# Optimization experiments

Measured on AMD Instinct MI355X. Metric: run time of the kernel, lower is better.

## Reference

```python
import jax, jax.numpy as jnp
import numpy as np

EPS = 1e-12  # matches torch F.normalize eps


def _l2_normalize(x):
    n = jnp.linalg.norm(x, axis=-1, keepdims=True)
    return x / jnp.maximum(n, EPS)


def setup_inputs() -> dict:
    key = jax.random.key(0)
    k1, k2, k3 = jax.random.split(key, 3)
    N, E, D = 100000, 1200000, 64
    feat = jax.random.normal(k1, (N, D), dtype=jnp.float32)
    beta = jnp.ones((1,), dtype=jnp.float32)
    src = jax.random.randint(k2, (E,), 0, N, dtype=jnp.int32)
    dst = jax.random.randint(k3, (E,), 0, N, dtype=jnp.int32)
    return {"feat": feat, "beta": beta, "src": src, "dst": dst}


def reference(feat, beta, src, dst):
    N = feat.shape[0]
    # cosine similarity on each edge (AGNN att_type)
    nh = _l2_normalize(feat)                                  # [N, D]
    e = beta[0] * jnp.sum(nh[src] * nh[dst], axis=-1)         # [E]
    # edge softmax over incoming edges of each destination node
    emax = jax.ops.segment_max(e, dst, num_segments=N)        # [N]
    emax = jnp.where(jnp.isfinite(emax), emax, 0.0)           # isolated nodes
    p = jnp.exp(e - emax[dst])                                # [E]
    psum = jax.ops.segment_sum(p, dst, num_segments=N)        # [N]
    p = p / jnp.maximum(psum[dst], EPS)                       # [E]
    # weighted scatter-sum aggregation: h_i' = sum_j p_ij * h_j
    msg = feat[src] * p[:, None]                              # [E, D]
    out = jax.ops.segment_sum(msg, dst, num_segments=N)       # [N, D]
    return out
```

## Files before the change

### kernel.cpp

```cpp
#include <hip/hip_runtime.h>
#include <hip/hip_fp16.h>

#define D 64
#define EPS 1e-12f
#define NPB 512
#define NPB_SHIFT 9
#define NB 256
#define CAP 8192
#define CAP_SHIFT 13
#define EPB 4096
#define SRC_BITS 17

typedef _Float16 hv2 __attribute__((ext_vector_type(2)));

__device__ inline unsigned bc_u(__half2 h) { return __builtin_bit_cast(unsigned, h); }
__device__ inline __half2  bc_h(unsigned u) { return __builtin_bit_cast(__half2, u); }

__device__ inline float fdot2f(unsigned a, unsigned b, float c) {
#if defined(__has_builtin) && __has_builtin(__builtin_amdgcn_fdot2)
    return __builtin_amdgcn_fdot2(__builtin_bit_cast(hv2, a),
                                  __builtin_bit_cast(hv2, b), c, false);
#else
    __half2 ah = bc_h(a), bh = bc_h(b);
    return c + __low2float(ah) * __low2float(bh)
             + __high2float(ah) * __high2float(bh);
#endif
}

__global__ __launch_bounds__(1024) void scatter_kernel(
        const int* __restrict__ src,
        const int* __restrict__ dst,
        int* __restrict__ bincursor,
        unsigned* __restrict__ pairs, int E) {
    __shared__ int hist[NB], offs[NB], cursor[NB], gbase[NB], tmp[NB];
    __shared__ int dstbuf[EPB];
    __shared__ unsigned buf[EPB];
    __shared__ unsigned char binof[EPB];

    int tid  = threadIdx.x;
    int base = blockIdx.x * EPB;
    int cnt  = min(EPB, E - base);

    if (tid < NB) hist[tid] = 0;
    __syncthreads();
    for (int i = tid; i < cnt; i += 1024) {
        int dd = dst[base + i];
        dstbuf[i] = dd;
        atomicAdd(&hist[dd >> NPB_SHIFT], 1);
    }
    __syncthreads();
    int v = 0;
    if (tid < NB) { v = hist[tid]; tmp[tid] = v; }
    __syncthreads();
    #pragma unroll
    for (int off = 1; off < NB; off <<= 1) {
        int t = 0;
        if (tid < NB && tid >= off) t = tmp[tid - off];
        __syncthreads();
        if (tid < NB) tmp[tid] += t;
        __syncthreads();
    }
    if (tid < NB) {
        int e = tmp[tid] - v;
        offs[tid] = e; cursor[tid] = e;
        if (v > 0)
            gbase[tid] = (tid << CAP_SHIFT) + atomicAdd(&bincursor[tid], v);
    }
    __syncthreads();
    for (int i = tid; i < cnt; i += 1024) {
        int s = src[base + i], dd = dstbuf[i];
        int b = dd >> NPB_SHIFT;
        int l = atomicAdd(&cursor[b], 1);
        buf[l]   = ((unsigned)(dd & (NPB - 1)) << SRC_BITS) | (unsigned)s;
        binof[l] = (unsigned char)b;
    }
    __syncthreads();
    for (int i = tid; i < cnt; i += 1024) {
        int b = binof[i];
        pairs[gbase[b] + (i - offs[b])] = buf[i];
    }
}

__global__ __launch_bounds__(1024) void csr_nh_kernel(
        const unsigned* __restrict__ pairs,
        const int* __restrict__ bincursor,
        int* __restrict__ rowbeg,
        int* __restrict__ rowend,
        int* __restrict__ esrc,
        const float4* __restrict__ feat4,
        float* __restrict__ norms,
        uint2* __restrict__ nh2,
        int N, int nbins) {
    __shared__ unsigned buf[CAP];
    __shared__ int hist[NPB], cursor[NPB], tmp[NPB];

    if ((int)blockIdx.x >= nbins) {
        int gid = (blockIdx.x - nbins) * 1024 + threadIdx.x;
        int row = gid >> 4;
        int lg  = gid & 15;
        if (row >= N) return;
        float4 v = feat4[row * 16 + lg];
        float ss = v.x * v.x + v.y * v.y + v.z * v.z + v.w * v.w;
        #pragma unroll
        for (int off = 1; off < 16; off <<= 1) ss += __shfl_xor(ss, off, 64);
        float nrm = fmaxf(sqrtf(ss), EPS);
        float inv = 1.0f / nrm;
        if (lg == 0) norms[row] = nrm;
        uint2 p;
        p.x = bc_u(__floats2half2_rn(v.x * inv, v.y * inv));
        p.y = bc_u(__floats2half2_rn(v.z * inv, v.w * inv));
        nh2[row * 16 + lg] = p;
        return;
    }

    int b    = blockIdx.x;
    int tid  = threadIdx.x;
    int base = b << CAP_SHIFT;
    int cnt  = bincursor[b];
    int node0 = b << NPB_SHIFT;

    if (tid < NPB) hist[tid] = 0;
    __syncthreads();
    for (int i = tid; i < cnt; i += 1024) {
        unsigned p = pairs[base + i];
        buf[i] = p;
        atomicAdd(&hist[p >> SRC_BITS], 1);
    }
    __syncthreads();
    int v = 0;
    if (tid < NPB) { v = hist[tid]; tmp[tid] = v; }
    __syncthreads();
    #pragma unroll
    for (int off = 1; off < NPB; off <<= 1) {
        int t = 0;
        if (tid < NPB && tid >= off) t = tmp[tid - off];
        __syncthreads();
        if (tid < NPB) tmp[tid] += t;
        __syncthreads();
    }
    if (tid < NPB) {
        int excl = tmp[tid] - v;
        cursor[tid] = excl;
        int node = node0 + tid;
        if (node < N) { rowbeg[node] = base + excl; rowend[node] = base + excl + v; }
    }
    __syncthreads();
    for (int i = tid; i < cnt; i += 1024) {
        unsigned p = buf[i];
        int pos = atomicAdd(&cursor[p >> SRC_BITS], 1);
        esrc[base + pos] = (int)(p & ((1u << SRC_BITS) - 1));
    }
}

__global__ __launch_bounds__(256) void gather_kernel(const uint4* __restrict__ nh4,
                                                     const float* __restrict__ norms,
                                                     const float* __restrict__ beta_p,
                                                     const int* __restrict__ rowbeg,
                                                     const int* __restrict__ rowend,
                                                     const int* __restrict__ esrc,
                                                     float4* __restrict__ out4, int N) {
    int t    = blockIdx.x * 256 + threadIdx.x;
    int lane = threadIdx.x & 63;
    int g    = lane >> 3;
    int lg   = lane & 7;
    int d    = (t >> 6) * 8 + g;
    if (d >= N) return;

    int j   = rowbeg[d];
    int end = rowend[d];
    float beta = beta_p[0];

    uint4 fdp = nh4[(size_t)d * 8 + lg];

    __half2 acc0 = __float2half2_rn(0.f), acc1 = acc0, acc2 = acc0, acc3 = acc0;
    float ps = 0.f;

    for (; j < end; j += 4) {
        bool v1 = (j + 1 < end), v2 = (j + 2 < end), v3 = (j + 3 < end);
        int s0 = esrc[j];
        int s1 = v1 ? esrc[j + 1] : s0;
        int s2 = v2 ? esrc[j + 2] : s0;
        int s3 = v3 ? esrc[j + 3] : s0;
        uint4 p0 = nh4[(size_t)s0 * 8 + lg];
        uint4 p1 = nh4[(size_t)s1 * 8 + lg];
        uint4 p2 = nh4[(size_t)s2 * 8 + lg];
        uint4 p3 = nh4[(size_t)s3 * 8 + lg];
        float n0 = norms[s0], n1 = norms[s1], n2 = norms[s2], n3 = norms[s3];
        float d0 = fdot2f(p0.x, fdp.x, 0.f), d1 = fdot2f(p1.x, fdp.x, 0.f);
        float d2 = fdot2f(p2.x, fdp.x, 0.f), d3 = fdot2f(p3.x, fdp.x, 0.f);
        d0 = fdot2f(p0.y, fdp.y, d0); d1 = fdot2f(p1.y, fdp.y, d1);
        d2 = fdot2f(p2.y, fdp.y, d2); d3 = fdot2f(p3.y, fdp.y, d3);
        d0 = fdot2f(p0.z, fdp.z, d0); d1 = fdot2f(p1.z, fdp.z, d1);
        d2 = fdot2f(p2.z, fdp.z, d2); d3 = fdot2f(p3.z, fdp.z, d3);
        d0 = fdot2f(p0.w, fdp.w, d0); d1 = fdot2f(p1.w, fdp.w, d1);
        d2 = fdot2f(p2.w, fdp.w, d2); d3 = fdot2f(p3.w, fdp.w, d3);
        #pragma unroll
        for (int off = 1; off < 8; off <<= 1) {
            d0 += __shfl_xor(d0, off, 64);
            d1 += __shfl_xor(d1, off, 64);
            d2 += __shfl_xor(d2, off, 64);
            d3 += __shfl_xor(d3, off, 64);
        }
        float w0 = __expf(beta * d0);
        float w1 = v1 ? __expf(beta * d1) : 0.f;
        float w2 = v2 ? __expf(beta * d2) : 0.f;
        float w3 = v3 ? __expf(beta * d3) : 0.f;
        __half2 q0 = __float2half2_rn(w0 * n0);
        __half2 q1 = __float2half2_rn(w1 * n1);
        __half2 q2 = __float2half2_rn(w2 * n2);
        __half2 q3 = __float2half2_rn(w3 * n3);
        acc0 = __hfma2(q0, bc_h(p0.x), acc0); acc0 = __hfma2(q1, bc_h(p1.x), acc0);
        acc0 = __hfma2(q2, bc_h(p2.x), acc0); acc0 = __hfma2(q3, bc_h(p3.x), acc0);
        acc1 = __hfma2(q0, bc_h(p0.y), acc1); acc1 = __hfma2(q1, bc_h(p1.y), acc1);
        acc1 = __hfma2(q2, bc_h(p2.y), acc1); acc1 = __hfma2(q3, bc_h(p3.y), acc1);
        acc2 = __hfma2(q0, bc_h(p0.z), acc2); acc2 = __hfma2(q1, bc_h(p1.z), acc2);
        acc2 = __hfma2(q2, bc_h(p2.z), acc2); acc2 = __hfma2(q3, bc_h(p3.z), acc2);
        acc3 = __hfma2(q0, bc_h(p0.w), acc3); acc3 = __hfma2(q1, bc_h(p1.w), acc3);
        acc3 = __hfma2(q2, bc_h(p2.w), acc3); acc3 = __hfma2(q3, bc_h(p3.w), acc3);
        ps += w0 + w1 + w2 + w3;
    }

    float r = 1.0f / fmaxf(ps, EPS);
    float4 o0 = {__low2float(acc0) * r, __high2float(acc0) * r,
                 __low2float(acc1) * r, __high2float(acc1) * r};
    float4 o1 = {__low2float(acc2) * r, __high2float(acc2) * r,
                 __low2float(acc3) * r, __high2float(acc3) * r};
    out4[(size_t)d * 16 + lg * 2]     = o0;
    out4[(size_t)d * 16 + lg * 2 + 1] = o1;
}

extern "C" void kernel_launch(void* const* d_in, const int* in_sizes, int n_in,
                              void* d_out, int out_size, void* d_ws, size_t ws_size,
                              hipStream_t stream) {
    const float* feat = (const float*)d_in[0];
    const float* beta = (const float*)d_in[1];
    const int*   src  = (const int*)d_in[2];
    const int*   dst  = (const int*)d_in[3];

    int N = in_sizes[0] / D;
    int E = in_sizes[2];
    int nbins = (N + NPB - 1) / NPB;

    unsigned* pairs     = (unsigned*)d_ws;
    int*      esrc      = (int*)(pairs + (size_t)nbins * CAP);
    unsigned* nhraw     = (unsigned*)(esrc + (size_t)nbins * CAP);
    float*    norms     = (float*)(nhraw + (size_t)N * 32);
    int*      bincursor = (int*)(norms + N);
    int*      rowbeg    = bincursor + NB;
    int*      rowend    = rowbeg + N;

    hipMemsetAsync(bincursor, 0, NB * sizeof(int), stream);

    int BS = (E + EPB - 1) / EPB;
    int BI = (N * 16 + 1023) / 1024;
    scatter_kernel<<<BS, 1024, 0, stream>>>(src, dst, bincursor, pairs, E);
    csr_nh_kernel<<<nbins + BI, 1024, 0, stream>>>(
        pairs, bincursor, rowbeg, rowend, esrc,
        (const float4*)feat, norms, (uint2*)nhraw, N, nbins);
    gather_kernel<<<(N + 31) / 32, 256, 0, stream>>>(
        (const uint4*)nhraw, norms, beta, rowbeg, rowend, esrc,
        (float4*)d_out, N);
}
```

Measured before the change: 135.1 us.

## Fuse three stages into one persistent kernel with grid barriers

```diff
diff --git a/kernel.cpp b/kernel.cpp
--- a/kernel.cpp
+++ b/kernel.cpp
@@ -10,6 +10,8 @@
 #define CAP_SHIFT 13
 #define EPB 4096
 #define SRC_BITS 17
+#define GB 256
+#define BT 1024
 
 typedef _Float16 hv2 __attribute__((ext_vector_type(2)));
 
@@ -27,206 +29,241 @@
 #endif
 }
 
-__global__ __launch_bounds__(1024) void scatter_kernel(
+struct SmemP1 {
+    int dstbuf[EPB];
+    unsigned buf[EPB];
+    int hist[NB], offs[NB], cursor[NB], gbase[NB];
+    unsigned char binof[EPB];
+};
+struct SmemP2 {
+    unsigned buf[CAP];
+    int hist[NPB], cursor[NPB];
+};
+constexpr size_t SMEM_BYTES = sizeof(SmemP1) > sizeof(SmemP2) ? sizeof(SmemP1)
+                                                              : sizeof(SmemP2);
+
+__device__ inline void grid_barrier(int* cnt, int target) {
+    __syncthreads();
+    if (threadIdx.x == 0) {
+        __threadfence();
+        atomicAdd(cnt, 1);
+        while (__hip_atomic_load(cnt, __ATOMIC_RELAXED, __HIP_MEMORY_SCOPE_AGENT)
+               < target)
+            __builtin_amdgcn_s_sleep(2);
+        __threadfence();
+    }
+    __syncthreads();
+}
+
+__global__ __launch_bounds__(BT) void fused_kernel(
         const int* __restrict__ src,
         const int* __restrict__ dst,
+        const float4* __restrict__ feat4,
+        const float* __restrict__ beta_p,
+        unsigned* __restrict__ pairs,
         int* __restrict__ bincursor,
-        unsigned* __restrict__ pairs, int E) {
-    __shared__ int hist[NB], offs[NB], cursor[NB], gbase[NB], tmp[NB];
-    __shared__ int dstbuf[EPB];
-    __shared__ unsigned buf[EPB];
-    __shared__ unsigned char binof[EPB];
-
-    int tid  = threadIdx.x;
-    int base = blockIdx.x * EPB;
-    int cnt  = min(EPB, E - base);
-
-    if (tid < NB) hist[tid] = 0;
-    __syncthreads();
-    for (int i = tid; i < cnt; i += 1024) {
-        int dd = dst[base + i];
-        dstbuf[i] = dd;
-        atomicAdd(&hist[dd >> NPB_SHIFT], 1);
-    }
-    __syncthreads();
-    int v = 0;
-    if (tid < NB) { v = hist[tid]; tmp[tid] = v; }
-    __syncthreads();
-    #pragma unroll
-    for (int off = 1; off < NB; off <<= 1) {
-        int t = 0;
-        if (tid < NB && tid >= off) t = tmp[tid - off];
-        __syncthreads();
-        if (tid < NB) tmp[tid] += t;
-        __syncthreads();
-    }
-    if (tid < NB) {
-        int e = tmp[tid] - v;
-        offs[tid] = e; cursor[tid] = e;
-        if (v > 0)
-            gbase[tid] = (tid << CAP_SHIFT) + atomicAdd(&bincursor[tid], v);
-    }
-    __syncthreads();
-    for (int i = tid; i < cnt; i += 1024) {
-        int s = src[base + i], dd = dstbuf[i];
-        int b = dd >> NPB_SHIFT;
-        int l = atomicAdd(&cursor[b], 1);
-        buf[l]   = ((unsigned)(dd & (NPB - 1)) << SRC_BITS) | (unsigned)s;
-        binof[l] = (unsigned char)b;
-    }
-    __syncthreads();
-    for (int i = tid; i < cnt; i += 1024) {
-        int b = binof[i];
-        pairs[gbase[b] + (i - offs[b])] = buf[i];
-    }
-}
-
-__global__ __launch_bounds__(1024) void csr_nh_kernel(
-        const unsigned* __restrict__ pairs,
-        const int* __restrict__ bincursor,
+        int* __restrict__ barcnt,
         int* __restrict__ rowbeg,
         int* __restrict__ rowend,
         int* __restrict__ esrc,
-        const float4* __restrict__ feat4,
         float* __restrict__ norms,
         uint2* __restrict__ nh2,
-        int N, int nbins) {
-    __shared__ unsigned buf[CAP];
-    __shared__ int hist[NPB], cursor[NPB], tmp[NPB];
-
-    if ((int)blockIdx.x >= nbins) {
-        int gid = (blockIdx.x - nbins) * 1024 + threadIdx.x;
-        int row = gid >> 4;
-        int lg  = gid & 15;
-        if (row >= N) return;
-        float4 v = feat4[row * 16 + lg];
-        float ss = v.x * v.x + v.y * v.y + v.z * v.z + v.w * v.w;
-        #pragma unroll
-        for (int off = 1; off < 16; off <<= 1) ss += __shfl_xor(ss, off, 64);
-        float nrm = fmaxf(sqrtf(ss), EPS);
-        float inv = 1.0f / nrm;
-        if (lg == 0) norms[row] = nrm;
-        uint2 p;
-        p.x = bc_u(__floats2half2_rn(v.x * inv, v.y * inv));
-        p.y = bc_u(__floats2half2_rn(v.z * inv, v.w * inv));
-        nh2[row * 16 + lg] = p;
-        return;
-    }
-
-    int b    = blockIdx.x;
-    int tid  = threadIdx.x;
-    int base = b << CAP_SHIFT;
-    int cnt  = bincursor[b];
-    int node0 = b << NPB_SHIFT;
-
-    if (tid < NPB) hist[tid] = 0;
-    __syncthreads();
-    for (int i = tid; i < cnt; i += 1024) {
-        unsigned p = pairs[base + i];
-        buf[i] = p;
-        atomicAdd(&hist[p >> SRC_BITS], 1);
-    }
-    __syncthreads();
-    int v = 0;
-    if (tid < NPB) { v = hist[tid]; tmp[tid] = v; }
-    __syncthreads();
-    #pragma unroll
-    for (int off = 1; off < NPB; off <<= 1) {
-        int t = 0;
-        if (tid < NPB && tid >= off) t = tmp[tid - off];
-        __syncthreads();
-        if (tid < NPB) tmp[tid] += t;
-        __syncthreads();
-    }
-    if (tid < NPB) {
-        int excl = tmp[tid] - v;
-        cursor[tid] = excl;
-        int node = node0 + tid;
-        if (node < N) { rowbeg[node] = base + excl; rowend[node] = base + excl + v; }
-    }
-    __syncthreads();
-    for (int i = tid; i < cnt; i += 1024) {
-        unsigned p = buf[i];
-        int pos = atomicAdd(&cursor[p >> SRC_BITS], 1);
-        esrc[base + pos] = (int)(p & ((1u << SRC_BITS) - 1));
-    }
-}
-
-__global__ __launch_bounds__(256) void gather_kernel(const uint4* __restrict__ nh4,
-                                                     const float* __restrict__ norms,
-                                                     const float* __restrict__ beta_p,
-                                                     const int* __restrict__ rowbeg,
-                                                     const int* __restrict__ rowend,
-                                                     const int* __restrict__ esrc,
-                                                     float4* __restrict__ out4, int N) {
-    int t    = blockIdx.x * 256 + threadIdx.x;
-    int lane = threadIdx.x & 63;
-    int g    = lane >> 3;
-    int lg   = lane & 7;
-    int d    = (t >> 6) * 8 + g;
-    if (d >= N) return;
-
-    int j   = rowbeg[d];
-    int end = rowend[d];
-    float beta = beta_p[0];
-
-    uint4 fdp = nh4[(size_t)d * 8 + lg];
-
-    __half2 acc0 = __float2half2_rn(0.f), acc1 = acc0, acc2 = acc0, acc3 = acc0;
-    float ps = 0.f;
-
-    for (; j < end; j += 4) {
-        bool v1 = (j + 1 < end), v2 = (j + 2 < end), v3 = (j + 3 < end);
-        int s0 = esrc[j];
-        int s1 = v1 ? esrc[j + 1] : s0;
-        int s2 = v2 ? esrc[j + 2] : s0;
-        int s3 = v3 ? esrc[j + 3] : s0;
-        uint4 p0 = nh4[(size_t)s0 * 8 + lg];
-        uint4 p1 = nh4[(size_t)s1 * 8 + lg];
-        uint4 p2 = nh4[(size_t)s2 * 8 + lg];
-        uint4 p3 = nh4[(size_t)s3 * 8 + lg];
-        float n0 = norms[s0], n1 = norms[s1], n2 = norms[s2], n3 = norms[s3];
-        float d0 = fdot2f(p0.x, fdp.x, 0.f), d1 = fdot2f(p1.x, fdp.x, 0.f);
-        float d2 = fdot2f(p2.x, fdp.x, 0.f), d3 = fdot2f(p3.x, fdp.x, 0.f);
-        d0 = fdot2f(p0.y, fdp.y, d0); d1 = fdot2f(p1.y, fdp.y, d1);
-        d2 = fdot2f(p2.y, fdp.y, d2); d3 = fdot2f(p3.y, fdp.y, d3);
-        d0 = fdot2f(p0.z, fdp.z, d0); d1 = fdot2f(p1.z, fdp.z, d1);
-        d2 = fdot2f(p2.z, fdp.z, d2); d3 = fdot2f(p3.z, fdp.z, d3);
-        d0 = fdot2f(p0.w, fdp.w, d0); d1 = fdot2f(p1.w, fdp.w, d1);
-        d2 = fdot2f(p2.w, fdp.w, d2); d3 = fdot2f(p3.w, fdp.w, d3);
-        #pragma unroll
-        for (int off = 1; off < 8; off <<= 1) {
-            d0 += __shfl_xor(d0, off, 64);
-            d1 += __shfl_xor(d1, off, 64);
-            d2 += __shfl_xor(d2, off, 64);
-            d3 += __shfl_xor(d3, off, 64);
-        }
-        float w0 = __expf(beta * d0);
-        float w1 = v1 ? __expf(beta * d1) : 0.f;
-        float w2 = v2 ? __expf(beta * d2) : 0.f;
-        float w3 = v3 ? __expf(beta * d3) : 0.f;
-        __half2 q0 = __float2half2_rn(w0 * n0);
-        __half2 q1 = __float2half2_rn(w1 * n1);
-        __half2 q2 = __float2half2_rn(w2 * n2);
-        __half2 q3 = __float2half2_rn(w3 * n3);
-        acc0 = __hfma2(q0, bc_h(p0.x), acc0); acc0 = __hfma2(q1, bc_h(p1.x), acc0);
-        acc0 = __hfma2(q2, bc_h(p2.x), acc0); acc0 = __hfma2(q3, bc_h(p3.x), acc0);
-        acc1 = __hfma2(q0, bc_h(p0.y), acc1); acc1 = __hfma2(q1, bc_h(p1.y), acc1);
-        acc1 = __hfma2(q2, bc_h(p2.y), acc1); acc1 = __hfma2(q3, bc_h(p3.y), acc1);
-        acc2 = __hfma2(q0, bc_h(p0.z), acc2); acc2 = __hfma2(q1, bc_h(p1.z), acc2);
-        acc2 = __hfma2(q2, bc_h(p2.z), acc2); acc2 = __hfma2(q3, bc_h(p3.z), acc2);
-        acc3 = __hfma2(q0, bc_h(p0.w), acc3); acc3 = __hfma2(q1, bc_h(p1.w), acc3);
-        acc3 = __hfma2(q2, bc_h(p2.w), acc3); acc3 = __hfma2(q3, bc_h(p3.w), acc3);
-        ps += w0 + w1 + w2 + w3;
-    }
-
-    float r = 1.0f / fmaxf(ps, EPS);
-    float4 o0 = {__low2float(acc0) * r, __high2float(acc0) * r,
-                 __low2float(acc1) * r, __high2float(acc1) * r};
-    float4 o1 = {__low2float(acc2) * r, __high2float(acc2) * r,
-                 __low2float(acc3) * r, __high2float(acc3) * r};
-    out4[(size_t)d * 16 + lg * 2]     = o0;
-    out4[(size_t)d * 16 + lg * 2 + 1] = o1;
+        float4* __restrict__ out4,
+        int N, int E, int nbins, int nchunks) {
+    __shared__ __align__(16) unsigned char smem[SMEM_BYTES];
+    SmemP1* s1 = (SmemP1*)smem;
+    SmemP2* s2 = (SmemP2*)smem;
+    const int tid = threadIdx.x;
+    const int bid = blockIdx.x;
+
+    for (int c = bid; c < nchunks; c += GB) {
+        int base = c * EPB;
+        int cnt  = min(EPB, E - base);
+        if (tid < NB) s1->hist[tid] = 0;
+        __syncthreads();
+        for (int i = tid; i < cnt; i += BT) {
+            int dd = dst[base + i];
+            s1->dstbuf[i] = dd;
+            atomicAdd(&s1->hist[dd >> NPB_SHIFT], 1);
+        }
+        __syncthreads();
+        if (tid < 64) {
+            int i0 = tid << 2;
+            int h0 = s1->hist[i0], h1 = s1->hist[i0 + 1];
+            int h2 = s1->hist[i0 + 2], h3 = s1->hist[i0 + 3];
+            int s = h0 + h1 + h2 + h3;
+            int run = s;
+            #pragma unroll
+            for (int off = 1; off < 64; off <<= 1) {
+                int nbr = __shfl_up(run, off, 64);
+                if (tid >= off) run += nbr;
+            }
+            int acc = run - s;
+            int hh[4] = {h0, h1, h2, h3};
+            #pragma unroll
+            for (int k = 0; k < 4; k++) {
+                s1->offs[i0 + k] = acc;
+                s1->cursor[i0 + k] = acc;
+                if (hh[k] > 0)
+                    s1->gbase[i0 + k] = ((i0 + k) << CAP_SHIFT)
+                                      + atomicAdd(&bincursor[i0 + k], hh[k]);
+                acc += hh[k];
+            }
+        }
+        __syncthreads();
+        for (int i = tid; i < cnt; i += BT) {
+            int s = src[base + i], dd = s1->dstbuf[i];
+            int b = dd >> NPB_SHIFT;
+            int l = atomicAdd(&s1->cursor[b], 1);
+            s1->buf[l]   = ((unsigned)(dd & (NPB - 1)) << SRC_BITS) | (unsigned)s;
+            s1->binof[l] = (unsigned char)b;
+        }
+        __syncthreads();
+        for (int i = tid; i < cnt; i += BT) {
+            int b = s1->binof[i];
+            pairs[s1->gbase[b] + (i - s1->offs[b])] = s1->buf[i];
+        }
+        __syncthreads();
+    }
+
+    {
+        const int stride = GB * BT;
+        for (int gid = bid * BT + tid; gid < N * 16; gid += stride) {
+            int row = gid >> 4, lg = gid & 15;
+            float4 v = feat4[gid];
+            float ss = v.x * v.x + v.y * v.y + v.z * v.z + v.w * v.w;
+            #pragma unroll
+            for (int off = 1; off < 16; off <<= 1) ss += __shfl_xor(ss, off, 64);
+            float nrm = fmaxf(sqrtf(ss), EPS);
+            float inv = 1.0f / nrm;
+            if (lg == 0) norms[row] = nrm;
+            uint2 p;
+            p.x = bc_u(__floats2half2_rn(v.x * inv, v.y * inv));
+            p.y = bc_u(__floats2half2_rn(v.z * inv, v.w * inv));
+            nh2[gid] = p;
+        }
+    }
+
+    grid_barrier(barcnt, GB);
+
+    for (int b = bid; b < nbins; b += GB) {
+        int base  = b << CAP_SHIFT;
+        int cnt   = bincursor[b];
+        int node0 = b << NPB_SHIFT;
+        if (tid < NPB) s2->hist[tid] = 0;
+        __syncthreads();
+        for (int i = tid; i < cnt; i += BT) {
+            unsigned p = pairs[base + i];
+            s2->buf[i] = p;
+            atomicAdd(&s2->hist[p >> SRC_BITS], 1);
+        }
+        __syncthreads();
+        if (tid < 64) {
+            int i0 = tid << 3;
+            int h[8], s = 0;
+            #pragma unroll
+            for (int k = 0; k < 8; k++) { h[k] = s2->hist[i0 + k]; s += h[k]; }
+            int run = s;
+            #pragma unroll
+            for (int off = 1; off < 64; off <<= 1) {
+                int nbr = __shfl_up(run, off, 64);
+                if (tid >= off) run += nbr;
+            }
+            int acc = run - s;
+            #pragma unroll
+            for (int k = 0; k < 8; k++) {
+                s2->cursor[i0 + k] = acc;
+                int node = node0 + i0 + k;
+                if (node < N) {
+                    rowbeg[node] = base + acc;
+                    rowend[node] = base + acc + h[k];
+                }
+                acc += h[k];
+            }
+        }
+        __syncthreads();
+        for (int i = tid; i < cnt; i += BT) {
+            unsigned p = s2->buf[i];
+            int pos = atomicAdd(&s2->cursor[p >> SRC_BITS], 1);
+            esrc[base + pos] = (int)(p & ((1u << SRC_BITS) - 1));
+        }
+        __syncthreads();
+    }
+
+    grid_barrier(barcnt, 2 * GB);
+
+    {
+        const uint4* nh4 = (const uint4*)nh2;
+        float beta = beta_p[0];
+        int lane = tid & 63;
+        int g  = lane >> 3;
+        int lg = lane & 7;
+        int wid = (bid << 4) + (tid >> 6);
+        const int nwaves = GB * (BT >> 6);
+        int ntasks = (N + 7) >> 3;
+        for (int task = wid; task < ntasks; task += nwaves) {
+            int d = task * 8 + g;
+            if (d >= N) continue;
+            int j   = rowbeg[d];
+            int end = rowend[d];
+            uint4 fdp = nh4[(size_t)d * 8 + lg];
+            __half2 acc0 = __float2half2_rn(0.f), acc1 = acc0;
+            __half2 acc2 = acc0, acc3 = acc0;
+            float ps = 0.f;
+            for (; j < end; j += 4) {
+                bool v1 = (j + 1 < end), v2 = (j + 2 < end), v3 = (j + 3 < end);
+                int es0 = esrc[j];
+                int es1 = v1 ? esrc[j + 1] : es0;
+                int es2 = v2 ? esrc[j + 2] : es0;
+                int es3 = v3 ? esrc[j + 3] : es0;
+                uint4 p0 = nh4[(size_t)es0 * 8 + lg];
+                uint4 p1 = nh4[(size_t)es1 * 8 + lg];
+                uint4 p2 = nh4[(size_t)es2 * 8 + lg];
+                uint4 p3 = nh4[(size_t)es3 * 8 + lg];
+                float n0 = norms[es0], n1 = norms[es1];
+                float n2 = norms[es2], n3 = norms[es3];
+                float d0 = fdot2f(p0.x, fdp.x, 0.f), d1 = fdot2f(p1.x, fdp.x, 0.f);
+                float d2 = fdot2f(p2.x, fdp.x, 0.f), d3 = fdot2f(p3.x, fdp.x, 0.f);
+                d0 = fdot2f(p0.y, fdp.y, d0); d1 = fdot2f(p1.y, fdp.y, d1);
+                d2 = fdot2f(p2.y, fdp.y, d2); d3 = fdot2f(p3.y, fdp.y, d3);
+                d0 = fdot2f(p0.z, fdp.z, d0); d1 = fdot2f(p1.z, fdp.z, d1);
+                d2 = fdot2f(p2.z, fdp.z, d2); d3 = fdot2f(p3.z, fdp.z, d3);
+                d0 = fdot2f(p0.w, fdp.w, d0); d1 = fdot2f(p1.w, fdp.w, d1);
+                d2 = fdot2f(p2.w, fdp.w, d2); d3 = fdot2f(p3.w, fdp.w, d3);
+                #pragma unroll
+                for (int off = 1; off < 8; off <<= 1) {
+                    d0 += __shfl_xor(d0, off, 64);
+                    d1 += __shfl_xor(d1, off, 64);
+                    d2 += __shfl_xor(d2, off, 64);
+                    d3 += __shfl_xor(d3, off, 64);
+                }
+                float w0 = __expf(beta * d0);
+                float w1 = v1 ? __expf(beta * d1) : 0.f;
+                float w2 = v2 ? __expf(beta * d2) : 0.f;
+                float w3 = v3 ? __expf(beta * d3) : 0.f;
+                __half2 q0 = __float2half2_rn(w0 * n0);
+                __half2 q1 = __float2half2_rn(w1 * n1);
+                __half2 q2 = __float2half2_rn(w2 * n2);
+                __half2 q3 = __float2half2_rn(w3 * n3);
+                acc0 = __hfma2(q0, bc_h(p0.x), acc0); acc0 = __hfma2(q1, bc_h(p1.x), acc0);
+                acc0 = __hfma2(q2, bc_h(p2.x), acc0); acc0 = __hfma2(q3, bc_h(p3.x), acc0);
+                acc1 = __hfma2(q0, bc_h(p0.y), acc1); acc1 = __hfma2(q1, bc_h(p1.y), acc1);
+                acc1 = __hfma2(q2, bc_h(p2.y), acc1); acc1 = __hfma2(q3, bc_h(p3.y), acc1);
+                acc2 = __hfma2(q0, bc_h(p0.z), acc2); acc2 = __hfma2(q1, bc_h(p1.z), acc2);
+                acc2 = __hfma2(q2, bc_h(p2.z), acc2); acc2 = __hfma2(q3, bc_h(p3.z), acc2);
+                acc3 = __hfma2(q0, bc_h(p0.w), acc3); acc3 = __hfma2(q1, bc_h(p1.w), acc3);
+                acc3 = __hfma2(q2, bc_h(p2.w), acc3); acc3 = __hfma2(q3, bc_h(p3.w), acc3);
+                ps += w0 + w1 + w2 + w3;
+            }
+            float r = 1.0f / fmaxf(ps, EPS);
+            float4 o0 = {__low2float(acc0) * r, __high2float(acc0) * r,
+                         __low2float(acc1) * r, __high2float(acc1) * r};
+            float4 o1 = {__low2float(acc2) * r, __high2float(acc2) * r,
+                         __low2float(acc3) * r, __high2float(acc3) * r};
+            out4[(size_t)d * 16 + lg * 2]     = o0;
+            out4[(size_t)d * 16 + lg * 2 + 1] = o1;
+        }
+    }
 }
 
 extern "C" void kernel_launch(void* const* d_in, const int* in_sizes, int n_in,
@@ -239,25 +276,23 @@
 
     int N = in_sizes[0] / D;
     int E = in_sizes[2];
-    int nbins = (N + NPB - 1) / NPB;
+    int nbins   = (N + NPB - 1) / NPB;
+    int nchunks = (E + EPB - 1) / EPB;
 
     unsigned* pairs     = (unsigned*)d_ws;
     int*      esrc      = (int*)(pairs + (size_t)nbins * CAP);
     unsigned* nhraw     = (unsigned*)(esrc + (size_t)nbins * CAP);
     float*    norms     = (float*)(nhraw + (size_t)N * 32);
     int*      bincursor = (int*)(norms + N);
-    int*      rowbeg    = bincursor + NB;
+    int*      barcnt    = bincursor + NB;
+    int*      rowbeg    = barcnt + 4;
     int*      rowend    = rowbeg + N;
 
-    hipMemsetAsync(bincursor, 0, NB * sizeof(int), stream);
-
-    int BS = (E + EPB - 1) / EPB;
-    int BI = (N * 16 + 1023) / 1024;
-    scatter_kernel<<<BS, 1024, 0, stream>>>(src, dst, bincursor, pairs, E);
-    csr_nh_kernel<<<nbins + BI, 1024, 0, stream>>>(
-        pairs, bincursor, rowbeg, rowend, esrc,
-        (const float4*)feat, norms, (uint2*)nhraw, N, nbins);
-    gather_kernel<<<(N + 31) / 32, 256, 0, stream>>>(
-        (const uint4*)nhraw, norms, beta, rowbeg, rowend, esrc,
-        (float4*)d_out, N);
-}
+    hipMemsetAsync(bincursor, 0, (NB + 4) * sizeof(int), stream);
+
+    fused_kernel<<<GB, BT, 0, stream>>>(
+        src, dst, (const float4*)feat, beta,
+        pairs, bincursor, barcnt, rowbeg, rowend, esrc,
+        norms, (uint2*)nhraw, (float4*)d_out,
+        N, E, nbins, nchunks);
+}
```

After: 213.4 us. +57.9%, slower.

## Fuse CSR build into gather via per-bin claim/done flags; merge nh into scatter

Applied to the files above, without the earlier changes.

```diff
diff --git a/kernel.cpp b/kernel.cpp
--- a/kernel.cpp
+++ b/kernel.cpp
@@ -10,6 +10,8 @@
 #define CAP_SHIFT 13
 #define EPB 4096
 #define SRC_BITS 17
+#define K2T 512
+#define NPBLK 64
 
 typedef _Float16 hv2 __attribute__((ext_vector_type(2)));
 
@@ -27,79 +29,26 @@
 #endif
 }
 
-__global__ __launch_bounds__(1024) void scatter_kernel(
+__global__ __launch_bounds__(1024) void scatter_nh_kernel(
         const int* __restrict__ src,
         const int* __restrict__ dst,
+        const float4* __restrict__ feat4,
         int* __restrict__ bincursor,
-        unsigned* __restrict__ pairs, int E) {
-    __shared__ int hist[NB], offs[NB], cursor[NB], gbase[NB], tmp[NB];
-    __shared__ int dstbuf[EPB];
-    __shared__ unsigned buf[EPB];
-    __shared__ unsigned char binof[EPB];
-
-    int tid  = threadIdx.x;
-    int base = blockIdx.x * EPB;
-    int cnt  = min(EPB, E - base);
-
-    if (tid < NB) hist[tid] = 0;
-    __syncthreads();
-    for (int i = tid; i < cnt; i += 1024) {
-        int dd = dst[base + i];
-        dstbuf[i] = dd;
-        atomicAdd(&hist[dd >> NPB_SHIFT], 1);
-    }
-    __syncthreads();
-    int v = 0;
-    if (tid < NB) { v = hist[tid]; tmp[tid] = v; }
-    __syncthreads();
-    #pragma unroll
-    for (int off = 1; off < NB; off <<= 1) {
-        int t = 0;
-        if (tid < NB && tid >= off) t = tmp[tid - off];
-        __syncthreads();
-        if (tid < NB) tmp[tid] += t;
-        __syncthreads();
-    }
-    if (tid < NB) {
-        int e = tmp[tid] - v;
-        offs[tid] = e; cursor[tid] = e;
-        if (v > 0)
-            gbase[tid] = (tid << CAP_SHIFT) + atomicAdd(&bincursor[tid], v);
-    }
-    __syncthreads();
-    for (int i = tid; i < cnt; i += 1024) {
-        int s = src[base + i], dd = dstbuf[i];
-        int b = dd >> NPB_SHIFT;
-        int l = atomicAdd(&cursor[b], 1);
-        buf[l]   = ((unsigned)(dd & (NPB - 1)) << SRC_BITS) | (unsigned)s;
-        binof[l] = (unsigned char)b;
-    }
-    __syncthreads();
-    for (int i = tid; i < cnt; i += 1024) {
-        int b = binof[i];
-        pairs[gbase[b] + (i - offs[b])] = buf[i];
-    }
-}
-
-__global__ __launch_bounds__(1024) void csr_nh_kernel(
-        const unsigned* __restrict__ pairs,
-        const int* __restrict__ bincursor,
-        int* __restrict__ rowbeg,
-        int* __restrict__ rowend,
-        int* __restrict__ esrc,
-        const float4* __restrict__ feat4,
+        unsigned* __restrict__ pairs,
         float* __restrict__ norms,
         uint2* __restrict__ nh2,
-        int N, int nbins) {
-    __shared__ unsigned buf[CAP];
-    __shared__ int hist[NPB], cursor[NPB], tmp[NPB];
-
-    if ((int)blockIdx.x >= nbins) {
-        int gid = (blockIdx.x - nbins) * 1024 + threadIdx.x;
-        int row = gid >> 4;
-        int lg  = gid & 15;
-        if (row >= N) return;
-        float4 v = feat4[row * 16 + lg];
+        int N, int E, int nchunks) {
+    __shared__ unsigned buf[EPB];
+    __shared__ int hist[NB], offs[NB], cursor[NB], gbase[NB];
+    __shared__ unsigned char binof[EPB];
+
+    int tid = threadIdx.x;
+
+    if ((int)blockIdx.x >= nchunks) {
+        int gid = (blockIdx.x - nchunks) * 1024 + tid;
+        if (gid >= N * 16) return;
+        int row = gid >> 4, lg = gid & 15;
+        float4 v = feat4[gid];
         float ss = v.x * v.x + v.y * v.y + v.z * v.z + v.w * v.w;
         #pragma unroll
         for (int off = 1; off < 16; off <<= 1) ss += __shfl_xor(ss, off, 64);
@@ -109,67 +58,173 @@
         uint2 p;
         p.x = bc_u(__floats2half2_rn(v.x * inv, v.y * inv));
         p.y = bc_u(__floats2half2_rn(v.z * inv, v.w * inv));
-        nh2[row * 16 + lg] = p;
+        nh2[gid] = p;
         return;
     }
 
-    int b    = blockIdx.x;
-    int tid  = threadIdx.x;
-    int base = b << CAP_SHIFT;
-    int cnt  = bincursor[b];
-    int node0 = b << NPB_SHIFT;
-
-    if (tid < NPB) hist[tid] = 0;
+    int base = blockIdx.x * EPB;
+    int cnt  = min(EPB, E - base);
+    int cnt4 = cnt >> 2;
+    int tail = cnt & 3;
+
+    if (tid < NB) hist[tid] = 0;
+    __syncthreads();
+
+    int4 dd4 = {0, 0, 0, 0};
+    bool have = tid < cnt4;
+    if (have) {
+        dd4 = ((const int4*)(dst + base))[tid];
+        atomicAdd(&hist[dd4.x >> NPB_SHIFT], 1);
+        atomicAdd(&hist[dd4.y >> NPB_SHIFT], 1);
+        atomicAdd(&hist[dd4.z >> NPB_SHIFT], 1);
+        atomicAdd(&hist[dd4.w >> NPB_SHIFT], 1);
+    }
+    int dtail = 0;
+    if (tid < tail) {
+        dtail = dst[base + cnt4 * 4 + tid];
+        atomicAdd(&hist[dtail >> NPB_SHIFT], 1);
+    }
+    __syncthreads();
+    if (tid < 64) {
+        int i0 = tid << 2;
+        int h0 = hist[i0], h1 = hist[i0 + 1], h2 = hist[i0 + 2], h3 = hist[i0 + 3];
+        int s = h0 + h1 + h2 + h3;
+        int run = s;
+        #pragma unroll
+        for (int off = 1; off < 64; off <<= 1) {
+            int nbr = __shfl_up(run, off, 64);
+            if (tid >= off) run += nbr;
+        }
+        int acc = run - s;
+        int hh[4] = {h0, h1, h2, h3};
+        #pragma unroll
+        for (int k = 0; k < 4; k++) {
+            offs[i0 + k] = acc;
+            cursor[i0 + k] = acc;
+            if (hh[k] > 0)
+                gbase[i0 + k] = ((i0 + k) << CAP_SHIFT)
+                              + atomicAdd(&bincursor[i0 + k], hh[k]);
+            acc += hh[k];
+        }
+    }
+    __syncthreads();
+    auto place = [&](int dd, int s) {
+        int bb = dd >> NPB_SHIFT;
+        int l = atomicAdd(&cursor[bb], 1);
+        buf[l]   = ((unsigned)(dd & (NPB - 1)) << SRC_BITS) | (unsigned)s;
+        binof[l] = (unsigned char)bb;
+    };
+    if (have) {
+        int4 ss4 = ((const int4*)(src + base))[tid];
+        place(dd4.x, ss4.x); place(dd4.y, ss4.y);
+        place(dd4.z, ss4.z); place(dd4.w, ss4.w);
+    }
+    if (tid < tail) place(dtail, src[base + cnt4 * 4 + tid]);
     __syncthreads();
     for (int i = tid; i < cnt; i += 1024) {
-        unsigned p = pairs[base + i];
-        buf[i] = p;
-        atomicAdd(&hist[p >> SRC_BITS], 1);
-    }
-    __syncthreads();
-    int v = 0;
-    if (tid < NPB) { v = hist[tid]; tmp[tid] = v; }
-    __syncthreads();
-    #pragma unroll
-    for (int off = 1; off < NPB; off <<= 1) {
-        int t = 0;
-        if (tid < NPB && tid >= off) t = tmp[tid - off];
-        __syncthreads();
-        if (tid < NPB) tmp[tid] += t;
-        __syncthreads();
-    }
-    if (tid < NPB) {
-        int excl = tmp[tid] - v;
-        cursor[tid] = excl;
-        int node = node0 + tid;
-        if (node < N) { rowbeg[node] = base + excl; rowend[node] = base + excl + v; }
-    }
-    __syncthreads();
-    for (int i = tid; i < cnt; i += 1024) {
-        unsigned p = buf[i];
-        int pos = atomicAdd(&cursor[p >> SRC_BITS], 1);
-        esrc[base + pos] = (int)(p & ((1u << SRC_BITS) - 1));
+        int b = binof[i];
+        pairs[gbase[b] + (i - offs[b])] = buf[i];
     }
 }
 
-__global__ __launch_bounds__(256) void gather_kernel(const uint4* __restrict__ nh4,
-                                                     const float* __restrict__ norms,
-                                                     const float* __restrict__ beta_p,
-                                                     const int* __restrict__ rowbeg,
-                                                     const int* __restrict__ rowend,
-                                                     const int* __restrict__ esrc,
-                                                     float4* __restrict__ out4, int N) {
-    int t    = blockIdx.x * 256 + threadIdx.x;
-    int lane = threadIdx.x & 63;
-    int g    = lane >> 3;
-    int lg   = lane & 7;
-    int d    = (t >> 6) * 8 + g;
+__global__ __launch_bounds__(K2T, 8) void csr_gather_kernel(
+        const unsigned* __restrict__ pairs,
+        const int* __restrict__ bincursor,
+        int* __restrict__ claim,
+        int* __restrict__ done,
+        int* __restrict__ rowbeg,
+        int* __restrict__ rowend,
+        int* __restrict__ esrc,
+        const uint4* __restrict__ nh4,
+        const float* __restrict__ norms,
+        const float* __restrict__ beta_p,
+        float4* __restrict__ out4, int N) {
+    __shared__ unsigned buf[CAP];
+    __shared__ int hist[NPB], cursor[NPB];
+    __shared__ int sclaim;
+
+    int tid   = threadIdx.x;
+    int node0 = blockIdx.x * NPBLK;
+    int b     = node0 >> NPB_SHIFT;
+
+    if (tid == 0) sclaim = atomicCAS(&claim[b], 0, 1);
+    __syncthreads();
+
+    if (sclaim == 0) {
+        int base = b << CAP_SHIFT;
+        int cnt  = bincursor[b];
+        int bn0  = b << NPB_SHIFT;
+        hist[tid] = 0;
+        __syncthreads();
+        int cnt4 = cnt >> 2;
+        for (int i4 = tid; i4 < cnt4; i4 += K2T) {
+            uint4 p = ((const uint4*)(pairs + base))[i4];
+            *(uint4*)&buf[i4 * 4] = p;
+            atomicAdd(&hist[p.x >> SRC_BITS], 1);
+            atomicAdd(&hist[p.y >> SRC_BITS], 1);
+            atomicAdd(&hist[p.z >> SRC_BITS], 1);
+            atomicAdd(&hist[p.w >> SRC_BITS], 1);
+        }
+        for (int i = cnt4 * 4 + tid; i < cnt; i += K2T) {
+            unsigned p = pairs[base + i];
+            buf[i] = p;
+            atomicAdd(&hist[p >> SRC_BITS], 1);
+        }
+        __syncthreads();
+        if (tid < 64) {
+            int i0 = tid << 3;
+            int h[8], s = 0;
+            #pragma unroll
+            for (int k = 0; k < 8; k++) { h[k] = hist[i0 + k]; s += h[k]; }
+            int run = s;
+            #pragma unroll
+            for (int off = 1; off < 64; off <<= 1) {
+                int nbr = __shfl_up(run, off, 64);
+                if (tid >= off) run += nbr;
+            }
+            int acc = run - s;
+            #pragma unroll
+            for (int k = 0; k < 8; k++) {
+                cursor[i0 + k] = acc;
+                int node = bn0 + i0 + k;
+                if (node < N) {
+                    rowbeg[node] = base + acc;
+                    rowend[node] = base + acc + h[k];
+                }
+                acc += h[k];
+            }
+        }
+        __syncthreads();
+        for (int i = tid; i < cnt; i += K2T) {
+            unsigned p = buf[i];
+            int pos = atomicAdd(&cursor[p >> SRC_BITS], 1);
+            esrc[base + pos] = (int)(p & ((1u << SRC_BITS) - 1));
+        }
+        __syncthreads();
+        if (tid == 0) {
+            __threadfence();
+            __hip_atomic_store(&done[b], 1, __ATOMIC_RELEASE,
+                               __HIP_MEMORY_SCOPE_AGENT);
+        }
+    } else {
+        if (tid == 0) {
+            while (__hip_atomic_load(&done[b], __ATOMIC_ACQUIRE,
+                                     __HIP_MEMORY_SCOPE_AGENT) == 0)
+                __builtin_amdgcn_s_sleep(2);
+            __threadfence();
+        }
+        __syncthreads();
+    }
+
+    int lane = tid & 63;
+    int g  = lane >> 3;
+    int lg = lane & 7;
+    int d  = node0 + (tid >> 6) * 8 + g;
     if (d >= N) return;
 
     int j   = rowbeg[d];
     int end = rowend[d];
     float beta = beta_p[0];
-
     uint4 fdp = nh4[(size_t)d * 8 + lg];
 
     __half2 acc0 = __float2half2_rn(0.f), acc1 = acc0, acc2 = acc0, acc3 = acc0;
@@ -239,25 +294,27 @@
 
     int N = in_sizes[0] / D;
     int E = in_sizes[2];
-    int nbins = (N + NPB - 1) / NPB;
+    int nbins   = (N + NPB - 1) / NPB;
+    int nchunks = (E + EPB - 1) / EPB;
 
     unsigned* pairs     = (unsigned*)d_ws;
     int*      esrc      = (int*)(pairs + (size_t)nbins * CAP);
     unsigned* nhraw     = (unsigned*)(esrc + (size_t)nbins * CAP);
     float*    norms     = (float*)(nhraw + (size_t)N * 32);
     int*      bincursor = (int*)(norms + N);
-    int*      rowbeg    = bincursor + NB;
+    int*      claim     = bincursor + NB;
+    int*      done      = claim + NB;
+    int*      rowbeg    = done + NB;
     int*      rowend    = rowbeg + N;
 
-    hipMemsetAsync(bincursor, 0, NB * sizeof(int), stream);
-
-    int BS = (E + EPB - 1) / EPB;
-    int BI = (N * 16 + 1023) / 1024;
-    scatter_kernel<<<BS, 1024, 0, stream>>>(src, dst, bincursor, pairs, E);
-    csr_nh_kernel<<<nbins + BI, 1024, 0, stream>>>(
-        pairs, bincursor, rowbeg, rowend, esrc,
-        (const float4*)feat, norms, (uint2*)nhraw, N, nbins);
-    gather_kernel<<<(N + 31) / 32, 256, 0, stream>>>(
-        (const uint4*)nhraw, norms, beta, rowbeg, rowend, esrc,
-        (float4*)d_out, N);
+    hipMemsetAsync(bincursor, 0, 3 * NB * sizeof(int), stream);
+
+    int BI  = (N * 16 + 1023) / 1024;
+    int BG2 = (N + NPBLK - 1) / NPBLK;
+    scatter_nh_kernel<<<nchunks + BI, 1024, 0, stream>>>(
+        src, dst, (const float4*)feat, bincursor, pairs, norms,
+        (uint2*)nhraw, N, E, nchunks);
+    csr_gather_kernel<<<BG2, K2T, 0, stream>>>(
+        pairs, bincursor, claim, done, rowbeg, rowend, esrc,
+        (const uint4*)nhraw, norms, beta, (float4*)d_out, N);
 }
```

Result: slower. 447.9 us (+231.4%).
